# Performance work log

Measured on AMD Instinct MI355X. Metric: run time of the kernel, lower is better.

The kernel has to match this reference:

```python
import jax, jax.numpy as jnp
import numpy as np

N = 50000
E = 800000
IN_DIM = 128
OUT_DIM = 128
NUM_HEADS = 4
HEAD_DIM = OUT_DIM // NUM_HEADS


def setup_inputs() -> dict:
    key = jax.random.key(0)
    ks = jax.random.split(key, 8)
    x = jax.random.normal(ks[0], (N, IN_DIM), dtype=jnp.float32)
    edge_index = jax.random.randint(ks[1], (2, E), 0, N, dtype=jnp.int64)
    # Linear(in_dim, out_dim, bias=False): store as [in, out] so h = x @ W
    s = 1.0 / np.sqrt(IN_DIM)
    W_src = jax.random.uniform(ks[2], (IN_DIM, OUT_DIM), jnp.float32, -s, s)
    W_dst = jax.random.uniform(ks[3], (IN_DIM, OUT_DIM), jnp.float32, -s, s)
    sa = 1.0 / np.sqrt(OUT_DIM)
    W_attn = jax.random.uniform(ks[4], (OUT_DIM, NUM_HEADS), jnp.float32, -sa, sa)
    ln_gamma = jnp.ones((OUT_DIM,), jnp.float32)
    ln_beta = jnp.zeros((OUT_DIM,), jnp.float32)
    return {"x": x, "edge_index": edge_index, "W_src": W_src, "W_dst": W_dst,
            "W_attn": W_attn, "ln_gamma": ln_gamma, "ln_beta": ln_beta}


def reference(x, edge_index, W_src, W_dst, W_attn, ln_gamma, ln_beta):
    n = x.shape[0]
    src_idx, dst_idx = edge_index[0], edge_index[1]
    h_src = x @ W_src                      # [N, OUT]
    h_dst = x @ W_dst                      # [N, OUT]
    hs_e = h_src[src_idx]                  # [E, OUT] gather
    a_input = hs_e + h_dst[dst_idx]        # [E, OUT]
    a = jax.nn.leaky_relu(a_input, negative_slope=0.2)
    alpha = a @ W_attn                     # [E, H]  (dropout is identity in eval)
    alpha_exp = jnp.exp(alpha - jnp.max(alpha))
    denom = jax.ops.segment_sum(alpha_exp, dst_idx, num_segments=n)  # [N, H]
    alpha_norm = alpha_exp / (denom[dst_idx] + 1e-9)                  # [E, H]
    msg = hs_e.reshape(-1, NUM_HEADS, HEAD_DIM) * alpha_norm[..., None]
    out = jax.ops.segment_sum(msg, dst_idx, num_segments=n)           # [N, H, D]
    out = out.reshape(n, OUT_DIM) + h_dst
    # LayerNorm over last dim
    mu = jnp.mean(out, axis=-1, keepdims=True)
    var = jnp.var(out, axis=-1, keepdims=True)
    return (out - mu) * jax.lax.rsqrt(var + 1e-5) * ln_gamma + ln_beta
```

## Files before the change

kernel.cpp:

```cpp
#include <hip/hip_runtime.h>
#include <hip/hip_bf16.h>
#include <math.h>

#define DIM 128
#define NHEADS 4
#define GROWS 16

__device__ __forceinline__ float bf2f(unsigned short u) {
    union { unsigned int i; float f; } v;
    v.i = ((unsigned int)u) << 16;
    return v.f;
}

__global__ __launch_bounds__(256) void k_dual_gemm(
    const float* __restrict__ x,
    const float* __restrict__ Wsrc, const float* __restrict__ Wdst,
    unsigned short* __restrict__ h_srcb, float* __restrict__ h_dst, int n)
{
    __shared__ float xs[GROWS][DIM];
    const int tid = threadIdx.x;
    const int r0 = blockIdx.x * GROWS;
    #pragma unroll
    for (int k = 0; k < GROWS * 32 / 256; ++k) {
        int idx = k * 256 + tid;
        int r = idx >> 5, c4 = idx & 31;
        int row = r0 + r;
        float4 v = make_float4(0.f, 0.f, 0.f, 0.f);
        if (row < n) v = ((const float4*)(x + (size_t)row * DIM))[c4];
        ((float4*)xs[r])[c4] = v;
    }
    __syncthreads();

    const int c = tid & 127;
    const bool is_src = (tid < 128);
    const float* __restrict__ W = is_src ? Wsrc : Wdst;

    float acc[GROWS];
    #pragma unroll
    for (int r = 0; r < GROWS; ++r) acc[r] = 0.f;

    #pragma unroll 2
    for (int j4 = 0; j4 < DIM / 4; ++j4) {
        const float w0 = W[(4 * j4 + 0) * DIM + c];
        const float w1 = W[(4 * j4 + 1) * DIM + c];
        const float w2 = W[(4 * j4 + 2) * DIM + c];
        const float w3 = W[(4 * j4 + 3) * DIM + c];
        #pragma unroll
        for (int r = 0; r < GROWS; ++r) {
            const float4 xv = ((const float4*)xs[r])[j4];
            acc[r] += xv.x * w0 + xv.y * w1 + xv.z * w2 + xv.w * w3;
        }
    }
    if (is_src) {
        #pragma unroll
        for (int r = 0; r < GROWS; ++r) {
            if (r0 + r < n) {
                __hip_bfloat16 b = __float2bfloat16(acc[r]);
                h_srcb[(size_t)(r0 + r) * DIM + c] = *(unsigned short*)&b;
            }
        }
    } else {
        #pragma unroll
        for (int r = 0; r < GROWS; ++r) {
            if (r0 + r < n) h_dst[(size_t)(r0 + r) * DIM + c] = acc[r];
        }
    }
}

__global__ __launch_bounds__(256) void k_hist(
    const int* __restrict__ ei, int* __restrict__ deg, int E)
{
    int e = blockIdx.x * 256 + threadIdx.x;
    if (e < E) atomicAdd(&deg[ei[E + e]], 1);
}

__global__ __launch_bounds__(1024) void k_scanA(
    const int* __restrict__ deg, int* __restrict__ exc,
    int* __restrict__ bsum, int n)
{
    __shared__ int buf[1024];
    const int t = threadIdx.x;
    const int i = blockIdx.x * 1024 + t;
    int v = (i < n) ? deg[i] : 0;
    buf[t] = v;
    __syncthreads();
    #pragma unroll
    for (int off = 1; off < 1024; off <<= 1) {
        int u = (t >= off) ? buf[t - off] : 0;
        __syncthreads();
        buf[t] += u;
        __syncthreads();
    }
    if (i < n) exc[i] = buf[t] - v;
    if (t == 1023) bsum[blockIdx.x] = buf[1023];
}

__global__ __launch_bounds__(1024) void k_scanB(int* __restrict__ bsum, int nb)
{
    __shared__ int buf[1024];
    const int t = threadIdx.x;
    int v = (t < nb) ? bsum[t] : 0;
    buf[t] = v;
    __syncthreads();
    #pragma unroll
    for (int off = 1; off < 1024; off <<= 1) {
        int u = (t >= off) ? buf[t - off] : 0;
        __syncthreads();
        buf[t] += u;
        __syncthreads();
    }
    if (t < nb) bsum[t] = buf[t] - v;
}

__global__ __launch_bounds__(256) void k_scanC(
    const int* __restrict__ exc, const int* __restrict__ bsum,
    int* __restrict__ offs, int* __restrict__ cursor, int n, int E)
{
    int i = blockIdx.x * 256 + threadIdx.x;
    if (i < n) {
        int o = exc[i] + bsum[i >> 10];
        offs[i] = o;
        cursor[i] = o;
    }
    if (i == 0) offs[n] = E;
}

__global__ __launch_bounds__(256) void k_scatter(
    const int* __restrict__ ei, int* __restrict__ cursor,
    int* __restrict__ srcs, int E)
{
    int e = blockIdx.x * 256 + threadIdx.x;
    if (e >= E) return;
    int s = ei[e];
    int d = ei[E + e];
    int pos = atomicAdd(&cursor[d], 1);
    srcs[pos] = s;
}

__global__ __launch_bounds__(256) void k_aggregate(
    const int* __restrict__ offs, const int* __restrict__ srcs,
    const unsigned short* __restrict__ h_srcb, const float* __restrict__ h_dst,
    const float* __restrict__ W_attn,
    const float* __restrict__ gamma, const float* __restrict__ beta,
    float* __restrict__ out, int n)
{
    const int node = blockIdx.x * 4 + (threadIdx.x >> 6);
    if (node >= n) return;
    const int lane = threadIdx.x & 63;
    const int half = lane >> 5;
    const int l    = lane & 31;
    const int head = l >> 3;

    const float4 hd = ((const float4*)(h_dst + (size_t)node * DIM))[l];

    const float4 w0 = ((const float4*)W_attn)[4 * l + 0];
    const float4 w1 = ((const float4*)W_attn)[4 * l + 1];
    const float4 w2 = ((const float4*)W_attn)[4 * l + 2];
    const float4 w3 = ((const float4*)W_attn)[4 * l + 3];

    const int beg = offs[node];
    const int end = offs[node + 1];

    float4 acc = make_float4(0.f, 0.f, 0.f, 0.f);
    float  den = 0.f;

    for (int j = beg + half; j < end; j += 2) {
        const int s = srcs[j];
        const ushort4 hu = ((const ushort4*)(h_srcb + (size_t)s * DIM))[l];
        const float hx = bf2f(hu.x), hy = bf2f(hu.y),
                    hz = bf2f(hu.z), hw = bf2f(hu.w);

        float a0 = hx + hd.x; a0 = a0 > 0.f ? a0 : 0.2f * a0;
        float a1 = hy + hd.y; a1 = a1 > 0.f ? a1 : 0.2f * a1;
        float a2 = hz + hd.z; a2 = a2 > 0.f ? a2 : 0.2f * a2;
        float a3 = hw + hd.w; a3 = a3 > 0.f ? a3 : 0.2f * a3;

        float px = a0 * w0.x + a1 * w1.x + a2 * w2.x + a3 * w3.x;
        float py = a0 * w0.y + a1 * w1.y + a2 * w2.y + a3 * w3.y;
        float pz = a0 * w0.z + a1 * w1.z + a2 * w2.z + a3 * w3.z;
        float pw = a0 * w0.w + a1 * w1.w + a2 * w2.w + a3 * w3.w;

        #pragma unroll
        for (int m = 16; m > 0; m >>= 1) {
            px += __shfl_xor(px, m, 32);
            py += __shfl_xor(py, m, 32);
            pz += __shfl_xor(pz, m, 32);
            pw += __shfl_xor(pw, m, 32);
        }

        const float ah = (head == 0) ? __expf(px) :
                         (head == 1) ? __expf(py) :
                         (head == 2) ? __expf(pz) : __expf(pw);

        acc.x += ah * hx;
        acc.y += ah * hy;
        acc.z += ah * hz;
        acc.w += ah * hw;
        den   += ah;
    }

    acc.x += __shfl_xor(acc.x, 32, 64);
    acc.y += __shfl_xor(acc.y, 32, 64);
    acc.z += __shfl_xor(acc.z, 32, 64);
    acc.w += __shfl_xor(acc.w, 32, 64);
    den   += __shfl_xor(den,   32, 64);

    const float dinv = 1.0f / (den + 1e-9f);
    float4 o;
    o.x = acc.x * dinv + hd.x;
    o.y = acc.y * dinv + hd.y;
    o.z = acc.z * dinv + hd.z;
    o.w = acc.w * dinv + hd.w;

    float s1 = o.x + o.y + o.z + o.w;
    float s2 = o.x * o.x + o.y * o.y + o.z * o.z + o.w * o.w;
    #pragma unroll
    for (int m = 16; m > 0; m >>= 1) {
        s1 += __shfl_xor(s1, m, 32);
        s2 += __shfl_xor(s2, m, 32);
    }
    const float mu   = s1 * (1.0f / 128.0f);
    const float var  = s2 * (1.0f / 128.0f) - mu * mu;
    const float rstd = rsqrtf(var + 1e-5f);

    if (half == 0) {
        const float4 g = ((const float4*)gamma)[l];
        const float4 b = ((const float4*)beta)[l];
        float4 res;
        res.x = (o.x - mu) * rstd * g.x + b.x;
        res.y = (o.y - mu) * rstd * g.y + b.y;
        res.z = (o.z - mu) * rstd * g.z + b.z;
        res.w = (o.w - mu) * rstd * g.w + b.w;
        ((float4*)(out + (size_t)node * DIM))[l] = res;
    }
}

extern "C" void kernel_launch(void* const* d_in, const int* in_sizes, int n_in,
                              void* d_out, int out_size, void* d_ws, size_t ws_size,
                              hipStream_t stream)
{
    const float* x     = (const float*)d_in[0];
    const int*   ei    = (const int*)d_in[1];
    const float* Wsrc  = (const float*)d_in[2];
    const float* Wdst  = (const float*)d_in[3];
    const float* Wattn = (const float*)d_in[4];
    const float* gamma = (const float*)d_in[5];
    const float* beta  = (const float*)d_in[6];
    float* out = (float*)d_out;

    const int n = in_sizes[0] / DIM;
    const int E = in_sizes[1] / 2;
    const int nb = (n + 1023) / 1024;

    float*          h_dst  = (float*)d_ws;
    unsigned short* h_srcb = (unsigned short*)(h_dst + (size_t)n * DIM);
    int*   deg    = (int*)(h_srcb + (size_t)n * DIM);
    int*   offs   = deg + n;
    int*   cursor = offs + n + 1;
    int*   srcs   = cursor + n;
    int*   exc    = srcs + E;
    int*   bsum   = exc + n;

    hipMemsetAsync(deg, 0, (size_t)n * sizeof(int), stream);

    k_hist <<<(E + 255) / 256, 256, 0, stream>>>(ei, deg, E);
    k_scanA<<<nb, 1024, 0, stream>>>(deg, exc, bsum, n);
    k_scanB<<<1, 1024, 0, stream>>>(bsum, nb);
    k_scanC<<<(n + 255) / 256, 256, 0, stream>>>(exc, bsum, offs, cursor, n, E);
    k_scatter<<<(E + 255) / 256, 256, 0, stream>>>(ei, cursor, srcs, E);

    k_dual_gemm<<<(n + GROWS - 1) / GROWS, 256, 0, stream>>>(x, Wsrc, Wdst, h_srcb, h_dst, n);

    k_aggregate<<<(n + 3) / 4, 256, 0, stream>>>(
        offs, srcs, h_srcb, h_dst, Wattn, gamma, beta, out, n);
}
```

Baseline: 359.9 us.

## Register-tile dual GEMM 4x4 per thread and cut shuffle reduction count

The projection GEMM now gives each thread a 4-row by 4-column tile. It reads weights as float4 and writes h_dst and the bf16 h_src as vector stores, replacing scalar per-column loads and stores. This raises arithmetic per load and coalesces the writes. In the edge-aggregation kernel, the four per-head butterfly reductions (20 shuffles) become a transpose-style reduction: pairs of head partials are exchanged and merged, so one value is reduced over the remaining steps and each lane picks its head with a final shuffle (8 shuffles). The shuffle count drops at the cost of extra selects and an added lane dependency.

```diff
diff --git a/kernel.cpp b/kernel.cpp
--- a/kernel.cpp
+++ b/kernel.cpp
@@ -21,7 +21,7 @@
     const int tid = threadIdx.x;
     const int r0 = blockIdx.x * GROWS;
     #pragma unroll
-    for (int k = 0; k < GROWS * 32 / 256; ++k) {
+    for (int k = 0; k < 2; ++k) {
         int idx = k * 256 + tid;
         int r = idx >> 5, c4 = idx & 31;
         int row = r0 + r;
@@ -31,38 +31,66 @@
     }
     __syncthreads();
 
-    const int c = tid & 127;
-    const bool is_src = (tid < 128);
+    const int tx = tid & 63;
+    const int ty = tid >> 6;
+    const bool is_src = (tx < 32);
     const float* __restrict__ W = is_src ? Wsrc : Wdst;
-
-    float acc[GROWS];
-    #pragma unroll
-    for (int r = 0; r < GROWS; ++r) acc[r] = 0.f;
+    const int c = (tx & 31) * 4;
+
+    float4 acc0 = make_float4(0.f,0.f,0.f,0.f);
+    float4 acc1 = make_float4(0.f,0.f,0.f,0.f);
+    float4 acc2 = make_float4(0.f,0.f,0.f,0.f);
+    float4 acc3 = make_float4(0.f,0.f,0.f,0.f);
 
     #pragma unroll 2
     for (int j4 = 0; j4 < DIM / 4; ++j4) {
-        const float w0 = W[(4 * j4 + 0) * DIM + c];
-        const float w1 = W[(4 * j4 + 1) * DIM + c];
-        const float w2 = W[(4 * j4 + 2) * DIM + c];
-        const float w3 = W[(4 * j4 + 3) * DIM + c];
-        #pragma unroll
-        for (int r = 0; r < GROWS; ++r) {
-            const float4 xv = ((const float4*)xs[r])[j4];
-            acc[r] += xv.x * w0 + xv.y * w1 + xv.z * w2 + xv.w * w3;
-        }
-    }
-    if (is_src) {
-        #pragma unroll
-        for (int r = 0; r < GROWS; ++r) {
-            if (r0 + r < n) {
-                __hip_bfloat16 b = __float2bfloat16(acc[r]);
-                h_srcb[(size_t)(r0 + r) * DIM + c] = *(unsigned short*)&b;
-            }
-        }
-    } else {
-        #pragma unroll
-        for (int r = 0; r < GROWS; ++r) {
-            if (r0 + r < n) h_dst[(size_t)(r0 + r) * DIM + c] = acc[r];
+        const float4 wv0 = *(const float4*)(W + (4*j4+0)*DIM + c);
+        const float4 wv1 = *(const float4*)(W + (4*j4+1)*DIM + c);
+        const float4 wv2 = *(const float4*)(W + (4*j4+2)*DIM + c);
+        const float4 wv3 = *(const float4*)(W + (4*j4+3)*DIM + c);
+
+        const float4 xv0 = ((const float4*)xs[ty*4+0])[j4];
+        const float4 xv1 = ((const float4*)xs[ty*4+1])[j4];
+        const float4 xv2 = ((const float4*)xs[ty*4+2])[j4];
+        const float4 xv3 = ((const float4*)xs[ty*4+3])[j4];
+
+        acc0.x += xv0.x*wv0.x + xv0.y*wv1.x + xv0.z*wv2.x + xv0.w*wv3.x;
+        acc0.y += xv0.x*wv0.y + xv0.y*wv1.y + xv0.z*wv2.y + xv0.w*wv3.y;
+        acc0.z += xv0.x*wv0.z + xv0.y*wv1.z + xv0.z*wv2.z + xv0.w*wv3.z;
+        acc0.w += xv0.x*wv0.w + xv0.y*wv1.w + xv0.z*wv2.w + xv0.w*wv3.w;
+
+        acc1.x += xv1.x*wv0.x + xv1.y*wv1.x + xv1.z*wv2.x + xv1.w*wv3.x;
+        acc1.y += xv1.x*wv0.y + xv1.y*wv1.y + xv1.z*wv2.y + xv1.w*wv3.y;
+        acc1.z += xv1.x*wv0.z + xv1.y*wv1.z + xv1.z*wv2.z + xv1.w*wv3.z;
+        acc1.w += xv1.x*wv0.w + xv1.y*wv1.w + xv1.z*wv2.w + xv1.w*wv3.w;
+
+        acc2.x += xv2.x*wv0.x + xv2.y*wv1.x + xv2.z*wv2.x + xv2.w*wv3.x;
+        acc2.y += xv2.x*wv0.y + xv2.y*wv1.y + xv2.z*wv2.y + xv2.w*wv3.y;
+        acc2.z += xv2.x*wv0.z + xv2.y*wv1.z + xv2.z*wv2.z + xv2.w*wv3.z;
+        acc2.w += xv2.x*wv0.w + xv2.y*wv1.w + xv2.z*wv2.w + xv2.w*wv3.w;
+
+        acc3.x += xv3.x*wv0.x + xv3.y*wv1.x + xv3.z*wv2.x + xv3.w*wv3.x;
+        acc3.y += xv3.x*wv0.y + xv3.y*wv1.y + xv3.z*wv2.y + xv3.w*wv3.y;
+        acc3.z += xv3.x*wv0.z + xv3.y*wv1.z + xv3.z*wv2.z + xv3.w*wv3.z;
+        acc3.w += xv3.x*wv0.w + xv3.y*wv1.w + xv3.z*wv2.w + xv3.w*wv3.w;
+    }
+
+    #pragma unroll
+    for (int rr = 0; rr < 4; ++rr) {
+        const int row = r0 + ty * 4 + rr;
+        if (row >= n) continue;
+        const float4 a = (rr == 0) ? acc0 : (rr == 1) ? acc1 : (rr == 2) ? acc2 : acc3;
+        if (is_src) {
+            __hip_bfloat16 b0 = __float2bfloat16(a.x);
+            __hip_bfloat16 b1 = __float2bfloat16(a.y);
+            __hip_bfloat16 b2 = __float2bfloat16(a.z);
+            __hip_bfloat16 b3 = __float2bfloat16(a.w);
+            ushort4 u;
+            u.x = *(unsigned short*)&b0; u.y = *(unsigned short*)&b1;
+            u.z = *(unsigned short*)&b2; u.w = *(unsigned short*)&b3;
+            *(ushort4*)(h_srcb + (size_t)row * DIM + c) = u;
+        } else {
+            *(float4*)(h_dst + (size_t)row * DIM + c) = a;
         }
     }
 }
@@ -180,17 +208,20 @@
         float pz = a0 * w0.z + a1 * w1.z + a2 * w2.z + a3 * w3.z;
         float pw = a0 * w0.w + a1 * w1.w + a2 * w2.w + a3 * w3.w;
 
-        #pragma unroll
-        for (int m = 16; m > 0; m >>= 1) {
-            px += __shfl_xor(px, m, 32);
-            py += __shfl_xor(py, m, 32);
-            pz += __shfl_xor(pz, m, 32);
-            pw += __shfl_xor(pw, m, 32);
-        }
-
-        const float ah = (head == 0) ? __expf(px) :
-                         (head == 1) ? __expf(py) :
-                         (head == 2) ? __expf(pz) : __expf(pw);
+        const bool b0_ = (l & 1);
+        float A = b0_ ? py : px;
+        A += __shfl_xor(b0_ ? px : py, 1, 32);
+        float B = b0_ ? pw : pz;
+        B += __shfl_xor(b0_ ? pz : pw, 1, 32);
+        const bool b1_ = (l & 2);
+        float Cv = b1_ ? B : A;
+        Cv += __shfl_xor(b1_ ? A : B, 2, 32);
+        Cv += __shfl_xor(Cv, 4, 32);
+        Cv += __shfl_xor(Cv, 8, 32);
+        Cv += __shfl_xor(Cv, 16, 32);
+        const float Sh = __shfl(Cv, head, 32);
+
+        const float ah = __expf(Sh);
 
         acc.x += ah * hx;
         acc.y += ah * hy;
```

Result: faster. 313.5 us (-12.9%).
